# Performance work log

Measured on AMD Instinct MI355X. Metric: run time of the kernel, lower is better.

Reference implementation:

```python
import jax, jax.numpy as jnp
import numpy as np

B, S, D = 2, 2048, 1024
H = 16
HD = D // H

def setup_inputs() -> dict:
    key = jax.random.key(0)
    ks = jax.random.split(key, 6)
    sc = 0.02
    return {
        'x': jax.random.normal(ks[0], (B, S, D), jnp.float32),
        'Wq': jax.random.normal(ks[1], (D, D), jnp.float32) * sc,
        'Wk': jax.random.normal(ks[2], (D, D), jnp.float32) * sc,
        'Wv': jax.random.normal(ks[3], (D, D), jnp.float32) * sc,
        'Wo': jax.random.normal(ks[4], (D, D), jnp.float32) * sc,
        'bo': jnp.zeros((D,), jnp.float32),
    }

def reference(x, Wq, Wk, Wv, Wo, bo):
    b, s, d_in = x.shape
    # torch Linear: y = x @ W.T
    q = jnp.einsum('bsd,ed->bse', x, Wq)
    k = jnp.einsum('bsd,ed->bse', x, Wk)
    v = jnp.einsum('bsd,ed->bse', x, Wv)
    # [b, h, s, hd]
    q = q.reshape(b, s, H, HD).transpose(0, 2, 1, 3)
    k = k.reshape(b, s, H, HD).transpose(0, 2, 1, 3)
    v = v.reshape(b, s, H, HD).transpose(0, 2, 1, 3)
    # NOTE: original divides by sqrt(d_out), not sqrt(head_dim)
    scores = jnp.einsum('bhqd,bhkd->bhqk', q, k) / jnp.sqrt(jnp.float32(D))
    causal = jnp.tril(jnp.ones((s, s), dtype=bool))  # True = keep
    scores = jnp.where(causal[None, None], scores, -jnp.inf)
    attn = jax.nn.softmax(scores, axis=-1)
    ctx = jnp.einsum('bhqk,bhkd->bhqd', attn, v)
    ctx = ctx.transpose(0, 2, 1, 3).reshape(b, s, D)
    return jnp.einsum('bsd,ed->bse', ctx, Wo) + bo
```

## Files before the change

kernel.cpp:

```cpp
#include <hip/hip_runtime.h>
#include <hip/hip_bf16.h>
#include <stdint.h>

typedef unsigned short u16;
typedef __attribute__((ext_vector_type(8))) short short8;
typedef __attribute__((ext_vector_type(4))) float f32x4;
typedef __attribute__((ext_vector_type(16))) float f32x16;
typedef __attribute__((ext_vector_type(4))) u16 u16x4;

#define NB 2
#define NS 2048
#define ND 1024
#define NH 16
#define NM 4096

#define QSCALE 0.045084220f

#if __has_builtin(__builtin_amdgcn_exp2f)
#define EXP2(x) __builtin_amdgcn_exp2f(x)
#else
#define EXP2(x) exp2f(x)
#endif
#if __has_builtin(__builtin_amdgcn_rcpf)
#define RCP(x) __builtin_amdgcn_rcpf(x)
#else
#define RCP(x) (1.0f / (x))
#endif

__device__ __forceinline__ u16 f2bf(float f){
  union { float f; unsigned u; } v; v.f = f;
  unsigned r = v.u + 0x7fff + ((v.u >> 16) & 1);
  return (u16)(r >> 16);
}

__device__ __forceinline__ unsigned cvtpk(float lo, float hi){
  unsigned r;
  asm("v_cvt_pk_bf16_f32 %0, %1, %2" : "=v"(r) : "v"(lo), "v"(hi));
  return r;
}

__device__ __forceinline__ void pl32swap(unsigned &e, unsigned &o){
  asm("v_permlane32_swap_b32 %0, %1" : "+v"(e), "+v"(o));
}

__device__ __forceinline__ void gload_lds16(const u16* g, u16* l){
  __builtin_amdgcn_global_load_lds(
      (const __attribute__((address_space(1))) unsigned int*)g,
      (__attribute__((address_space(3))) unsigned int*)l, 16, 0, 0);
}

__device__ __forceinline__ f32x16 mfma32(short8 a, short8 b, f32x16 c){
  return __builtin_amdgcn_mfma_f32_32x32x16_bf16(a, b, c, 0, 0, 0);
}

__global__ void cvt_kernel(const float* __restrict__ src, u16* __restrict__ dst, int n){
  int i = (blockIdx.x * blockDim.x + threadIdx.x) * 4;
  if (i < n){
    float4 v = *(const float4*)(src + i);
    u16x4 o = { f2bf(v.x), f2bf(v.y), f2bf(v.z), f2bf(v.w) };
    *(u16x4*)(dst + i) = o;
  }
}

__global__ void cvt4_kernel(const float* __restrict__ a, const float* __restrict__ b,
                            const float* __restrict__ c, const float* __restrict__ d,
                            u16* __restrict__ oa, u16* __restrict__ ob,
                            u16* __restrict__ oc, u16* __restrict__ od){
  const float* s; u16* o;
  switch (blockIdx.y){
    case 0: s = a; o = oa; break;
    case 1: s = b; o = ob; break;
    case 2: s = c; o = oc; break;
    default: s = d; o = od; break;
  }
  int i = (blockIdx.x * blockDim.x + threadIdx.x) * 4;
  float4 v = *(const float4*)(s + i);
  u16x4 pk = { f2bf(v.x), f2bf(v.y), f2bf(v.z), f2bf(v.w) };
  *(u16x4*)(o + i) = pk;
}

__device__ __forceinline__ void gemm_core(
    const u16* __restrict__ A, const u16* __restrict__ W,
    int m0, int n0, u16* lsA, u16* lsB, f32x4 acc[4][4])
{
  const int tid = threadIdx.x;
  const int l   = tid & 63;
  const int wr  = (tid >> 7) & 1;
  const int wc  = (tid >> 6) & 1;
  const int lr  = l & 15;
  const int lkb = (l >> 4) << 4;
  const int sr  = tid >> 3;
  const int scb = (tid & 7) << 4;

  for (int kt = 0; kt < 16; ++kt){
    const int k0 = kt << 6;
    #pragma unroll
    for (int i = 0; i < 4; ++i){
      int r   = (i << 5) + sr;
      int cbs = scb ^ ((r & 7) << 4);
      gload_lds16(&A[(size_t)(m0 + r) * ND + k0 + (cbs >> 1)], &lsA[r * 64 + (scb >> 1)]);
      gload_lds16(&W[(size_t)(n0 + r) * ND + k0 + (cbs >> 1)], &lsB[r * 64 + (scb >> 1)]);
    }
    __syncthreads();

    short8 af[4][2], bf[4][2];
    #pragma unroll
    for (int m16 = 0; m16 < 4; ++m16){
      int r  = (wr << 6) + (m16 << 4) + lr;
      int rx = (r & 7) << 4;
      #pragma unroll
      for (int ks = 0; ks < 2; ++ks){
        int off = r * 128 + (((ks << 6) + lkb) ^ rx);
        af[m16][ks] = *(const short8*)((const char*)lsA + off);
      }
    }
    #pragma unroll
    for (int n16 = 0; n16 < 4; ++n16){
      int r  = (wc << 6) + (n16 << 4) + lr;
      int rx = (r & 7) << 4;
      #pragma unroll
      for (int ks = 0; ks < 2; ++ks){
        int off = r * 128 + (((ks << 6) + lkb) ^ rx);
        bf[n16][ks] = *(const short8*)((const char*)lsB + off);
      }
    }
    #pragma unroll
    for (int m16 = 0; m16 < 4; ++m16)
      #pragma unroll
      for (int n16 = 0; n16 < 4; ++n16){
        acc[m16][n16] = __builtin_amdgcn_mfma_f32_16x16x32_bf16(af[m16][0], bf[n16][0], acc[m16][n16], 0, 0, 0);
        acc[m16][n16] = __builtin_amdgcn_mfma_f32_16x16x32_bf16(af[m16][1], bf[n16][1], acc[m16][n16], 0, 0, 0);
      }
    __syncthreads();
  }
}

__global__ __launch_bounds__(256) void gemm_qkv(
    const u16* __restrict__ xb,
    const u16* __restrict__ Wqb, const u16* __restrict__ Wkb, const u16* __restrict__ Wvb,
    u16* __restrict__ Qo, u16* __restrict__ Ko, u16* __restrict__ Vt)
{
  __shared__ u16 lsA[128*64];
  __shared__ u16 lsB[128*64];
  const int z = blockIdx.z;
  const u16* W = (z == 0) ? Wqb : (z == 1) ? Wkb : Wvb;
  const int m0 = blockIdx.x << 7, n0 = blockIdx.y << 7;
  f32x4 acc[4][4] = {};
  gemm_core(xb, W, m0, n0, lsA, lsB, acc);

  const int l  = threadIdx.x & 63;
  const int wr = (threadIdx.x >> 7) & 1, wc = (threadIdx.x >> 6) & 1;
  const int rb = m0 + (wr << 6) + ((l >> 4) << 2);
  const int cb = n0 + (wc << 6) + (l & 15);

  if (z < 2){
    const float sc = (z == 0) ? QSCALE : 1.0f;
    u16* C = (z == 0) ? Qo : Ko;
    #pragma unroll
    for (int m16 = 0; m16 < 4; ++m16)
      #pragma unroll
      for (int n16 = 0; n16 < 4; ++n16)
        #pragma unroll
        for (int r = 0; r < 4; ++r)
          C[(size_t)(rb + (m16 << 4) + r) * ND + cb + (n16 << 4)] = f2bf(acc[m16][n16][r] * sc);
  } else {
    #pragma unroll
    for (int m16 = 0; m16 < 4; ++m16){
      int srow = rb + (m16 << 4);
      int bi = srow >> 11, s = srow & 2047;
      #pragma unroll
      for (int n16 = 0; n16 < 4; ++n16){
        int col = cb + (n16 << 4);
        u16x4 pk = { f2bf(acc[m16][n16][0]), f2bf(acc[m16][n16][1]),
                     f2bf(acc[m16][n16][2]), f2bf(acc[m16][n16][3]) };
        *(u16x4*)&Vt[((size_t)(bi * 16 + (col >> 6)) * 64 + (col & 63)) * 2048 + s] = pk;
      }
    }
  }
}

__global__ __launch_bounds__(256) void gemm_out(
    const u16* __restrict__ ctxb, const u16* __restrict__ Wob,
    const float* __restrict__ bo, float* __restrict__ out)
{
  __shared__ u16 lsA[128*64];
  __shared__ u16 lsB[128*64];
  const int m0 = blockIdx.x << 7, n0 = blockIdx.y << 7;
  f32x4 acc[4][4] = {};
  gemm_core(ctxb, Wob, m0, n0, lsA, lsB, acc);

  const int l  = threadIdx.x & 63;
  const int wr = (threadIdx.x >> 7) & 1, wc = (threadIdx.x >> 6) & 1;
  const int rb = m0 + (wr << 6) + ((l >> 4) << 2);
  const int cb = n0 + (wc << 6) + (l & 15);
  #pragma unroll
  for (int m16 = 0; m16 < 4; ++m16)
    #pragma unroll
    for (int n16 = 0; n16 < 4; ++n16)
      #pragma unroll
      for (int r = 0; r < 4; ++r){
        int col = cb + (n16 << 4);
        out[(size_t)(rb + (m16 << 4) + r) * ND + col] = acc[m16][n16][r] + bo[col];
      }
}

__device__ __forceinline__ void stage_tile(const u16* src, int srcStride, u16* lds, int tid){
  const int rl = tid >> 3;
  const int ch = tid & 7;
  const int cs = ch ^ (rl & 7);
  gload_lds16(&src[(size_t)rl * srcStride + cs * 8],        &lds[rl * 64 + ch * 8]);
  gload_lds16(&src[(size_t)(rl + 32) * srcStride + cs * 8], &lds[(rl + 32) * 64 + ch * 8]);
}

__global__ __launch_bounds__(256) void attn_kernel(
    const u16* __restrict__ Q, const u16* __restrict__ K,
    const u16* __restrict__ Vt, u16* __restrict__ ctx)
{
  __shared__ __align__(16) u16 lsK[2][64*64];
  __shared__ __align__(16) u16 lsV[2][64*64];

  const int bid = blockIdx.x;
  const int xcd = bid & 7;
  const int j   = bid >> 3;
  const int bh  = xcd + 8 * (j >> 4);
  const int st  = 15 - (j & 15);
  const int b = bh >> 4, h = bh & 15;
  const int tid = threadIdx.x;
  const int l = tid & 63, w = tid >> 6;
  const int q5 = l & 31, hi = l >> 5;
  const int qb   = st * 128 + w * 32;
  const int qgl  = qb + q5;
  const int qmax = qb + 31;
  const int tb   = 2 * st + 1;

  const u16* Kb0 = &K[(size_t)(b * NS) * ND + h * 64];
  const u16* Vb0 = &Vt[(size_t)bh * 64 * NS];

  short8 qf[4];
  {
    const u16* Qrow = &Q[(size_t)(b * NS + qgl) * ND + h * 64 + hi * 8];
    #pragma unroll
    for (int ks = 0; ks < 4; ++ks)
      qf[ks] = *(const short8*)&Qrow[ks * 16];
  }

  float m_r = -3e38f, l_r = 0.f;
  f32x16 accA = {}, accB = {};

  int cur = 0;
  stage_tile(Kb0, ND, &lsK[0][0], tid);
  stage_tile(Vb0, NS, &lsV[0][0], tid);
  __syncthreads();

  #pragma unroll 1
  for (int t = 0; t <= tb; ++t){
    if (t < tb){
      stage_tile(&Kb0[(size_t)(t + 1) * 64 * ND], ND, &lsK[cur ^ 1][0], tid);
      stage_tile(&Vb0[(t + 1) * 64],              NS, &lsV[cur ^ 1][0], tid);
    }
    if (t * 64 <= qmax){
      const char* Kc = (const char*)&lsK[cur][0];
      const char* Vc = (const char*)&lsV[cur][0];
      const int swz = q5 & 7;

      f32x16 s0 = {}, s1 = {};
      #pragma unroll
      for (int ks = 0; ks < 4; ++ks){
        int c0 = ((2 * ks + hi) ^ swz) << 4;
        short8 k0 = *(const short8*)(Kc + q5 * 128 + c0);
        short8 k1 = *(const short8*)(Kc + (q5 + 32) * 128 + c0);
        s0 = mfma32(k0, qf[ks], s0);
        s1 = mfma32(k1, qf[ks], s1);
      }

      if (t * 64 + 63 > qb){
        #pragma unroll
        for (int r = 0; r < 16; ++r){
          int kl = t * 64 + (r & 3) + 8 * (r >> 2) + 4 * hi;
          if (kl > qgl)      s0[r] = -3e38f;
          if (kl + 32 > qgl) s1[r] = -3e38f;
        }
      }

      float mx[16];
      #pragma unroll
      for (int r = 0; r < 16; ++r) mx[r] = fmaxf(s0[r], s1[r]);
      #pragma unroll
      for (int stp = 8; stp > 0; stp >>= 1)
        #pragma unroll
        for (int r = 0; r < stp; ++r) mx[r] = fmaxf(mx[r], mx[r + stp]);
      float pm = fmaxf(mx[0], __shfl_xor(mx[0], 32));

      if (__any(pm > m_r + 8.f)){
        float mn = fmaxf(m_r, pm);
        float e  = EXP2(m_r - mn);
        m_r = mn; l_r *= e;
        #pragma unroll
        for (int r = 0; r < 16; ++r){ accA[r] *= e; accB[r] *= e; }
      }

      #pragma unroll
      for (int r = 0; r < 16; ++r){
        s0[r] = EXP2(s0[r] - m_r);
        s1[r] = EXP2(s1[r] - m_r);
      }
      float sm[16];
      #pragma unroll
      for (int r = 0; r < 16; ++r) sm[r] = s0[r] + s1[r];
      #pragma unroll
      for (int stp = 8; stp > 0; stp >>= 1)
        #pragma unroll
        for (int r = 0; r < stp; ++r) sm[r] += sm[r + stp];
      l_r += sm[0] + __shfl_xor(sm[0], 32);

      unsigned pw[2][4][2];
      #pragma unroll
      for (int g = 0; g < 4; ++g){
        pw[0][g][0] = cvtpk(s0[4*g],     s0[4*g + 1]);
        pw[0][g][1] = cvtpk(s0[4*g + 2], s0[4*g + 3]);
        pw[1][g][0] = cvtpk(s1[4*g],     s1[4*g + 1]);
        pw[1][g][1] = cvtpk(s1[4*g + 2], s1[4*g + 3]);
      }
      #pragma unroll
      for (int m = 0; m < 2; ++m)
        #pragma unroll
        for (int kp = 0; kp < 2; ++kp)
          #pragma unroll
          for (int i = 0; i < 2; ++i)
            pl32swap(pw[m][2*kp][i], pw[m][2*kp + 1][i]);

      #pragma unroll
      for (int ks = 0; ks < 4; ++ks){
        const int m = ks >> 1, kp = ks & 1;
        union { unsigned u[4]; short8 s8; } pa;
        pa.u[0] = pw[m][2*kp][0];
        pa.u[1] = pw[m][2*kp][1];
        pa.u[2] = pw[m][2*kp + 1][0];
        pa.u[3] = pw[m][2*kp + 1][1];
        int c0 = ((2 * ks + hi) ^ swz) << 4;
        short8 v0 = *(const short8*)(Vc + q5 * 128 + c0);
        short8 v1 = *(const short8*)(Vc + (q5 + 32) * 128 + c0);
        accA = mfma32(pa.s8, v0, accA);
        accB = mfma32(pa.s8, v1, accB);
      }
    }
    __syncthreads();
    cur ^= 1;
  }

  float inv = RCP(l_r);
  #pragma unroll
  for (int r = 0; r < 16; ++r){
    int qrow = (r & 3) + 8 * (r >> 2) + 4 * hi;
    float iv = __shfl(inv, (l & 32) | qrow, 64);
    u16* crow = &ctx[(size_t)(b * NS + qb + qrow) * ND + h * 64 + q5];
    crow[0]  = f2bf(accA[r] * iv);
    crow[32] = f2bf(accB[r] * iv);
  }
}

extern "C" void kernel_launch(void* const* d_in, const int* in_sizes, int n_in,
                              void* d_out, int out_size, void* d_ws, size_t ws_size,
                              hipStream_t stream)
{
  const float* x  = (const float*)d_in[0];
  const float* Wq = (const float*)d_in[1];
  const float* Wk = (const float*)d_in[2];
  const float* Wv = (const float*)d_in[3];
  const float* Wo = (const float*)d_in[4];
  const float* bo = (const float*)d_in[5];
  float* out = (float*)d_out;
  char* ws = (char*)d_ws;

  u16* xb  = (u16*)(ws);
  u16* Wqb = (u16*)(ws + (8u  << 20));
  u16* Wkb = (u16*)(ws + (10u << 20));
  u16* Wvb = (u16*)(ws + (12u << 20));
  u16* Wob = (u16*)(ws + (14u << 20));
  u16* Qb  = (u16*)(ws + (16u << 20));
  u16* Kb  = (u16*)(ws + (24u << 20));
  u16* Vtb = (u16*)(ws + (32u << 20));
  u16* Cb  = (u16*)(ws + (40u << 20));

  cvt_kernel<<<4096, 256, 0, stream>>>(x, xb, NM * ND);
  cvt4_kernel<<<dim3(1024, 4), 256, 0, stream>>>(Wq, Wk, Wv, Wo, Wqb, Wkb, Wvb, Wob);

  gemm_qkv<<<dim3(32, 8, 3), 256, 0, stream>>>(xb, Wqb, Wkb, Wvb, Qb, Kb, Vtb);
  attn_kernel<<<512, 256, 0, stream>>>(Qb, Kb, Vtb, Cb);
  gemm_out<<<dim3(32, 8), 256, 0, stream>>>(Cb, Wob, bo, out);
}
```

Baseline: 136.5 us.

## Software-pipeline attention with triple-buffered LDS and QK of next tile overlapping softmax

Restructures the attention loop so the QK^T MFMAs for tile t+1 are issued before the softmax and PV of tile t, using ping-pong score registers and a 2x manual unroll. K/V staging moves to a three-deep LDS ring so loads run two tiles ahead. MFMA sections are wrapped in s_setprio and launch bounds request two blocks per CU. This adds register pressure and LDS use, which could lower occupancy or cause spills.

```diff
diff --git a/kernel.cpp b/kernel.cpp
--- a/kernel.cpp
+++ b/kernel.cpp
@@ -19,7 +19,12 @@
 #if __has_builtin(__builtin_amdgcn_exp2f)
 #define EXP2(x) __builtin_amdgcn_exp2f(x)
 #else
-#define EXP2(x) exp2f(x)
+__device__ __forceinline__ float __exp2_asm(float x){
+  float r;
+  asm("v_exp_f32 %0, %1" : "=v"(r) : "v"(x));
+  return r;
+}
+#define EXP2(x) __exp2_asm(x)
 #endif
 #if __has_builtin(__builtin_amdgcn_rcpf)
 #define RCP(x) __builtin_amdgcn_rcpf(x)
@@ -212,12 +217,108 @@
   gload_lds16(&src[(size_t)(rl + 32) * srcStride + cs * 8], &lds[(rl + 32) * 64 + ch * 8]);
 }
 
-__global__ __launch_bounds__(256) void attn_kernel(
+__device__ __forceinline__ void qk_tile(const u16* lsKt, const short8 qf[4],
+                                        int q5, int hi, f32x16 &s0, f32x16 &s1){
+  const char* Kc = (const char*)lsKt;
+  const int swz = q5 & 7;
+  f32x16 a = {}, b = {};
+  __builtin_amdgcn_s_setprio(1);
+  #pragma unroll
+  for (int ks = 0; ks < 4; ++ks){
+    int c0 = ((2 * ks + hi) ^ swz) << 4;
+    short8 k0 = *(const short8*)(Kc + q5 * 128 + c0);
+    short8 k1 = *(const short8*)(Kc + (q5 + 32) * 128 + c0);
+    a = mfma32(k0, qf[ks], a);
+    b = mfma32(k1, qf[ks], b);
+  }
+  __builtin_amdgcn_s_setprio(0);
+  s0 = a; s1 = b;
+}
+
+__device__ __forceinline__ void sm_pv(f32x16 s0, f32x16 s1, const u16* lsVt,
+                                      int t, int qb, int qgl, int q5, int hi,
+                                      float &m_r, float &l_r, f32x16 &accA, f32x16 &accB){
+  if (t * 64 + 63 > qb){
+    #pragma unroll
+    for (int r = 0; r < 16; ++r){
+      int kl = t * 64 + (r & 3) + 8 * (r >> 2) + 4 * hi;
+      if (kl > qgl)      s0[r] = -3e38f;
+      if (kl + 32 > qgl) s1[r] = -3e38f;
+    }
+  }
+  float mx[16];
+  #pragma unroll
+  for (int r = 0; r < 16; ++r) mx[r] = fmaxf(s0[r], s1[r]);
+  #pragma unroll
+  for (int stp = 8; stp > 0; stp >>= 1)
+    #pragma unroll
+    for (int r = 0; r < stp; ++r) mx[r] = fmaxf(mx[r], mx[r + stp]);
+  float pm = fmaxf(mx[0], __shfl_xor(mx[0], 32));
+
+  if (__any(pm > m_r + 8.f)){
+    float mn = fmaxf(m_r, pm);
+    float e  = EXP2(m_r - mn);
+    m_r = mn; l_r *= e;
+    #pragma unroll
+    for (int r = 0; r < 16; ++r){ accA[r] *= e; accB[r] *= e; }
+  }
+
+  #pragma unroll
+  for (int r = 0; r < 16; ++r){
+    s0[r] = EXP2(s0[r] - m_r);
+    s1[r] = EXP2(s1[r] - m_r);
+  }
+  float sm[16];
+  #pragma unroll
+  for (int r = 0; r < 16; ++r) sm[r] = s0[r] + s1[r];
+  #pragma unroll
+  for (int stp = 8; stp > 0; stp >>= 1)
+    #pragma unroll
+    for (int r = 0; r < stp; ++r) sm[r] += sm[r + stp];
+  l_r += sm[0] + __shfl_xor(sm[0], 32);
+
+  unsigned pw[2][4][2];
+  #pragma unroll
+  for (int g = 0; g < 4; ++g){
+    pw[0][g][0] = cvtpk(s0[4*g],     s0[4*g + 1]);
+    pw[0][g][1] = cvtpk(s0[4*g + 2], s0[4*g + 3]);
+    pw[1][g][0] = cvtpk(s1[4*g],     s1[4*g + 1]);
+    pw[1][g][1] = cvtpk(s1[4*g + 2], s1[4*g + 3]);
+  }
+  #pragma unroll
+  for (int m = 0; m < 2; ++m)
+    #pragma unroll
+    for (int kp = 0; kp < 2; ++kp)
+      #pragma unroll
+      for (int i = 0; i < 2; ++i)
+        pl32swap(pw[m][2*kp][i], pw[m][2*kp + 1][i]);
+
+  const char* Vc = (const char*)lsVt;
+  const int swz = q5 & 7;
+  __builtin_amdgcn_s_setprio(1);
+  #pragma unroll
+  for (int ks = 0; ks < 4; ++ks){
+    const int m = ks >> 1, kp = ks & 1;
+    union { unsigned u[4]; short8 s8; } pa;
+    pa.u[0] = pw[m][2*kp][0];
+    pa.u[1] = pw[m][2*kp][1];
+    pa.u[2] = pw[m][2*kp + 1][0];
+    pa.u[3] = pw[m][2*kp + 1][1];
+    int c0 = ((2 * ks + hi) ^ swz) << 4;
+    short8 v0 = *(const short8*)(Vc + q5 * 128 + c0);
+    short8 v1 = *(const short8*)(Vc + (q5 + 32) * 128 + c0);
+    accA = mfma32(pa.s8, v0, accA);
+    accB = mfma32(pa.s8, v1, accB);
+  }
+  __builtin_amdgcn_s_setprio(0);
+}
+
+__global__ __launch_bounds__(256, 2) void attn_kernel(
     const u16* __restrict__ Q, const u16* __restrict__ K,
     const u16* __restrict__ Vt, u16* __restrict__ ctx)
 {
-  __shared__ __align__(16) u16 lsK[2][64*64];
-  __shared__ __align__(16) u16 lsV[2][64*64];
+  __shared__ __align__(16) u16 lsK[3][64*64];
+  __shared__ __align__(16) u16 lsV[3][64*64];
 
   const int bid = blockIdx.x;
   const int xcd = bid & 7;
@@ -230,7 +331,7 @@
   const int q5 = l & 31, hi = l >> 5;
   const int qb   = st * 128 + w * 32;
   const int qgl  = qb + q5;
-  const int qmax = qb + 31;
+  const int nc   = (qb + 31) >> 6;
   const int tb   = 2 * st + 1;
 
   const u16* Kb0 = &K[(size_t)(b * NS) * ND + h * 64];
@@ -246,106 +347,38 @@
 
   float m_r = -3e38f, l_r = 0.f;
   f32x16 accA = {}, accB = {};
-
-  int cur = 0;
-  stage_tile(Kb0, ND, &lsK[0][0], tid);
-  stage_tile(Vb0, NS, &lsV[0][0], tid);
+  f32x16 sA0, sA1, sB0, sB1;
+
+  stage_tile(Kb0, ND, lsK[0], tid);
+  stage_tile(Vb0, NS, lsV[0], tid);
+  stage_tile(&Kb0[(size_t)64 * ND], ND, lsK[1], tid);
+  stage_tile(&Vb0[64],              NS, lsV[1], tid);
   __syncthreads();
+  qk_tile(lsK[0], qf, q5, hi, sA0, sA1);
 
   #pragma unroll 1
-  for (int t = 0; t <= tb; ++t){
-    if (t < tb){
-      stage_tile(&Kb0[(size_t)(t + 1) * 64 * ND], ND, &lsK[cur ^ 1][0], tid);
-      stage_tile(&Vb0[(t + 1) * 64],              NS, &lsV[cur ^ 1][0], tid);
-    }
-    if (t * 64 <= qmax){
-      const char* Kc = (const char*)&lsK[cur][0];
-      const char* Vc = (const char*)&lsV[cur][0];
-      const int swz = q5 & 7;
-
-      f32x16 s0 = {}, s1 = {};
-      #pragma unroll
-      for (int ks = 0; ks < 4; ++ks){
-        int c0 = ((2 * ks + hi) ^ swz) << 4;
-        short8 k0 = *(const short8*)(Kc + q5 * 128 + c0);
-        short8 k1 = *(const short8*)(Kc + (q5 + 32) * 128 + c0);
-        s0 = mfma32(k0, qf[ks], s0);
-        s1 = mfma32(k1, qf[ks], s1);
-      }
-
-      if (t * 64 + 63 > qb){
-        #pragma unroll
-        for (int r = 0; r < 16; ++r){
-          int kl = t * 64 + (r & 3) + 8 * (r >> 2) + 4 * hi;
-          if (kl > qgl)      s0[r] = -3e38f;
-          if (kl + 32 > qgl) s1[r] = -3e38f;
-        }
-      }
-
-      float mx[16];
-      #pragma unroll
-      for (int r = 0; r < 16; ++r) mx[r] = fmaxf(s0[r], s1[r]);
-      #pragma unroll
-      for (int stp = 8; stp > 0; stp >>= 1)
-        #pragma unroll
-        for (int r = 0; r < stp; ++r) mx[r] = fmaxf(mx[r], mx[r + stp]);
-      float pm = fmaxf(mx[0], __shfl_xor(mx[0], 32));
-
-      if (__any(pm > m_r + 8.f)){
-        float mn = fmaxf(m_r, pm);
-        float e  = EXP2(m_r - mn);
-        m_r = mn; l_r *= e;
-        #pragma unroll
-        for (int r = 0; r < 16; ++r){ accA[r] *= e; accB[r] *= e; }
-      }
-
-      #pragma unroll
-      for (int r = 0; r < 16; ++r){
-        s0[r] = EXP2(s0[r] - m_r);
-        s1[r] = EXP2(s1[r] - m_r);
-      }
-      float sm[16];
-      #pragma unroll
-      for (int r = 0; r < 16; ++r) sm[r] = s0[r] + s1[r];
-      #pragma unroll
-      for (int stp = 8; stp > 0; stp >>= 1)
-        #pragma unroll
-        for (int r = 0; r < stp; ++r) sm[r] += sm[r + stp];
-      l_r += sm[0] + __shfl_xor(sm[0], 32);
-
-      unsigned pw[2][4][2];
-      #pragma unroll
-      for (int g = 0; g < 4; ++g){
-        pw[0][g][0] = cvtpk(s0[4*g],     s0[4*g + 1]);
-        pw[0][g][1] = cvtpk(s0[4*g + 2], s0[4*g + 3]);
-        pw[1][g][0] = cvtpk(s1[4*g],     s1[4*g + 1]);
-        pw[1][g][1] = cvtpk(s1[4*g + 2], s1[4*g + 3]);
-      }
-      #pragma unroll
-      for (int m = 0; m < 2; ++m)
-        #pragma unroll
-        for (int kp = 0; kp < 2; ++kp)
-          #pragma unroll
-          for (int i = 0; i < 2; ++i)
-            pl32swap(pw[m][2*kp][i], pw[m][2*kp + 1][i]);
-
-      #pragma unroll
-      for (int ks = 0; ks < 4; ++ks){
-        const int m = ks >> 1, kp = ks & 1;
-        union { unsigned u[4]; short8 s8; } pa;
-        pa.u[0] = pw[m][2*kp][0];
-        pa.u[1] = pw[m][2*kp][1];
-        pa.u[2] = pw[m][2*kp + 1][0];
-        pa.u[3] = pw[m][2*kp + 1][1];
-        int c0 = ((2 * ks + hi) ^ swz) << 4;
-        short8 v0 = *(const short8*)(Vc + q5 * 128 + c0);
-        short8 v1 = *(const short8*)(Vc + (q5 + 32) * 128 + c0);
-        accA = mfma32(pa.s8, v0, accA);
-        accB = mfma32(pa.s8, v1, accB);
-      }
-    }
-    __syncthreads();
-    cur ^= 1;
+  for (int t = 0; t <= tb; t += 2){
+    {
+      const int rs = (t + 2) % 3, rn = (t + 1) % 3, rc = t % 3;
+      if (t + 2 <= tb){
+        stage_tile(&Kb0[(size_t)(t + 2) * 64 * ND], ND, lsK[rs], tid);
+        stage_tile(&Vb0[(t + 2) * 64],              NS, lsV[rs], tid);
+      }
+      if (t + 1 <= nc) qk_tile(lsK[rn], qf, q5, hi, sB0, sB1);
+      if (t <= nc)     sm_pv(sA0, sA1, lsV[rc], t, qb, qgl, q5, hi, m_r, l_r, accA, accB);
+      __syncthreads();
+    }
+    {
+      const int t1 = t + 1;
+      const int rs = (t1 + 2) % 3, rn = (t1 + 1) % 3, rc = t1 % 3;
+      if (t1 + 2 <= tb){
+        stage_tile(&Kb0[(size_t)(t1 + 2) * 64 * ND], ND, lsK[rs], tid);
+        stage_tile(&Vb0[(t1 + 2) * 64],              NS, lsV[rs], tid);
+      }
+      if (t1 + 1 <= nc) qk_tile(lsK[rn], qf, q5, hi, sA0, sA1);
+      if (t1 <= nc)     sm_pv(sB0, sB1, lsV[rc], t1, qb, qgl, q5, hi, m_r, l_r, accA, accB);
+      __syncthreads();
+    }
   }
 
   float inv = RCP(l_r);
```

New measurement: 133.8 us. -2.0%, faster.
